# Kernel optimization log

Hardware: AMD Instinct MI355X
Metric: run time of the kernel (lower is better)

## Reference

```python
import jax, jax.numpy as jnp
import numpy as np

LAMBDA_MIN = 0.1
LAMBDA_GLOBAL_MIN = 0.1
LAMBDA_GLOBAL_SCALE = 1.0
SLOPE = 0.2  # negative_slope


def leaky(x):
    return jnp.where(x >= 0, x, SLOPE * x)


def setup_inputs() -> dict:
    key = jax.random.key(0)
    ks = jax.random.split(key, 16)
    n, d, E, C, R = 10000, 128, 320000, 50000, 20
    s = 0.05
    h = jax.random.normal(ks[0], (n, d), jnp.float32)
    edge_index = jax.random.randint(ks[1], (2, E), 0, n)
    edge_type = jax.random.randint(ks[2], (E,), 0, R)
    rel_table = jax.random.normal(ks[3], (R, d), jnp.float32) * s
    # constraints taken from a subset of edges so matches exist
    constraint_indices = edge_index[:, :C]
    constraint_values = jax.random.normal(ks[4], (C,), jnp.float32)
    constraint_types = jax.random.randint(ks[5], (C,), 0, 4)
    att_in = 3 * d  # out*2 + in_dim (use_relation)
    W = jax.random.normal(ks[6], (d, d), jnp.float32) * s
    W_bi = jax.random.normal(ks[7], (d, d), jnp.float32) * s
    att_w1 = jax.random.normal(ks[8], (d, att_in), jnp.float32) * s
    att_b1 = jnp.zeros((d,), jnp.float32)
    att_w2 = jax.random.normal(ks[9], (d,), jnp.float32) * s
    gate_w1 = jax.random.normal(ks[10], (d, 2 * d), jnp.float32) * s
    gate_b1 = jnp.zeros((d,), jnp.float32)
    gate_w2 = jax.random.normal(ks[11], (d,), jnp.float32) * s
    gate_b2 = jnp.zeros((), jnp.float32)
    lambda_c = jnp.full((4,), 0.5, jnp.float32)  # CONSTRAINT_LAMBDA_INIT
    lambda_global = jnp.array(0.5, jnp.float32)
    return dict(h=h, edge_index=edge_index, edge_type=edge_type,
                rel_table=rel_table, constraint_indices=constraint_indices,
                constraint_values=constraint_values, constraint_types=constraint_types,
                W=W, W_bi=W_bi, att_w1=att_w1, att_b1=att_b1, att_w2=att_w2,
                gate_w1=gate_w1, gate_b1=gate_b1, gate_w2=gate_w2, gate_b2=gate_b2,
                lambda_c=lambda_c, lambda_global=lambda_global)


def reference(h, edge_index, edge_type, rel_table, constraint_indices,
              constraint_values, constraint_types, W, W_bi, att_w1, att_b1,
              att_w2, gate_w1, gate_b1, gate_w2, gate_b2, lambda_c, lambda_global):
    n = h.shape[0]
    Wh = h @ W.T                                  # [n, d]
    src, tgt = edge_index[0], edge_index[1]
    src_emb, tgt_emb = Wh[src], Wh[tgt]           # [E, d]
    r_emb = rel_table[edge_type]                  # [E, d]
    att_in = jnp.concatenate([src_emb, tgt_emb, r_emb], axis=-1)  # [E, 3d]
    e = leaky(att_in @ att_w1.T + att_b1) @ att_w2                # [E]

    # ---- constraints (bounded lambdas) ----
    lc = jax.nn.sigmoid(lambda_c) * (1.0 - LAMBDA_MIN) + LAMBDA_MIN
    lg = jax.nn.sigmoid(lambda_global) * (LAMBDA_GLOBAL_SCALE - LAMBDA_GLOBAL_MIN) + LAMBDA_GLOBAL_MIN
    ws = lc[constraint_types] * constraint_values                 # [C]
    c_keys = constraint_indices[0] * n + constraint_indices[1]
    e_keys = src * n + tgt
    # O(n^2) scatter buffers, faithful to the original
    c_agg = jnp.zeros((n * n,), jnp.float32).at[c_keys].add(ws)
    c_exists = jnp.zeros((n * n,), jnp.float32).at[c_keys].add(1.0)
    ms = c_agg[e_keys]
    mask = c_exists[e_keys] > 0
    ms = ms * mask.astype(jnp.float32)
    # constraint gate on matched edges (unmatched entries are 0 anyway)
    gi = jnp.concatenate([src_emb, tgt_emb], axis=-1)             # [E, 2d]
    g = jax.nn.sigmoid(leaky(gi @ gate_w1.T + gate_b1) @ gate_w2 + gate_b2)
    ms = jnp.where(mask, g * ms, ms)
    n_matched = mask.sum()
    global_bias = lg * jnp.mean(ws) * 0.01
    e = jnp.where(n_matched > 0, e + lg * ms, e + global_bias)

    # ---- scatter softmax over src neighborhoods ----
    mx = jax.ops.segment_max(e, src, num_segments=n)
    ex = jnp.exp(jnp.minimum(e - mx[src], 20.0))
    sm = jax.ops.segment_sum(ex, src, num_segments=n)
    attn = ex / (sm[src] + 1e-10)                                 # [E]

    # ---- weighted scatter-add aggregation ----
    side = jax.ops.segment_sum(attn[:, None] * tgt_emb, src, num_segments=n)  # [n, d]

    sum_out = leaky(Wh + side)
    bi_out = leaky((Wh * side) @ W_bi.T)
    h_new = sum_out + bi_out + Wh   # bi-interaction + residual
    return jax.nn.elu(h_new)
```

## Files before the change

### kernel.cpp

```cpp
#include <hip/hip_runtime.h>
#include <stdint.h>

#define SLOPE 0.2f
#define HASH_SIZE 131072
#define POIS ((int)0xAAAAAAAA)
#define MAXDEG 64

typedef __attribute__((ext_vector_type(8))) short bf16x8;
typedef __attribute__((ext_vector_type(4))) float f32x4;

__device__ __forceinline__ float leakyf(float x) { return fmaxf(x, SLOPE * x); }
__device__ __forceinline__ float sigmoidf(float x) { return 1.f / (1.f + __expf(-x)); }
__device__ __forceinline__ unsigned short f2bf(float f) {
  union { float f; unsigned int i; } c; c.f = f;
  unsigned int u = c.i;
  return (unsigned short)((u + 0x7fffu + ((u >> 16) & 1u)) >> 16);
}
__device__ __forceinline__ float bf2f(unsigned short u) {
  union { unsigned int i; float f; } c; c.i = ((unsigned int)u) << 16; return c.f;
}
__device__ __forceinline__ void unpk8(uint4 v, float* o) {
  union { unsigned int i; float f; } t;
  t.i = v.x << 16;          o[0] = t.f;
  t.i = v.x & 0xffff0000u;  o[1] = t.f;
  t.i = v.y << 16;          o[2] = t.f;
  t.i = v.y & 0xffff0000u;  o[3] = t.f;
  t.i = v.z << 16;          o[4] = t.f;
  t.i = v.z & 0xffff0000u;  o[5] = t.f;
  t.i = v.w << 16;          o[6] = t.f;
  t.i = v.w & 0xffff0000u;  o[7] = t.f;
}
__device__ __forceinline__ void ldbf8(const unsigned short* p, float* o) {
  unpk8(*(const uint4*)p, o);
}

__device__ __forceinline__ void mfma_core_a(const bf16x8 (&afr)[4],
                                            const unsigned short* bptr, f32x4 (&acc)[8]) {
  #pragma unroll
  for (int ks = 0; ks < 4; ++ks) {
    #pragma unroll
    for (int ct = 0; ct < 8; ++ct) {
      bf16x8 b = *(const bf16x8*)(bptr + ct * 2048 + ks * 32);
      acc[ct] = __builtin_amdgcn_mfma_f32_16x16x32_bf16(afr[ks], b, acc[ct], 0, 0, 0);
    }
  }
}

__global__ __launch_bounds__(256) void setup_kernel(
    const float* __restrict__ aw1, const float* __restrict__ gw1,
    const float* __restrict__ W, const float* __restrict__ Wbi,
    const float* __restrict__ rel, const float* __restrict__ ab1,
    const int* __restrict__ cidx, const float* __restrict__ cval,
    const int* __restrict__ ctype, const float* __restrict__ lc,
    unsigned short* __restrict__ Wcat, unsigned short* __restrict__ P3b16,
    int* __restrict__ hkeys,
    int C, int n, int R, int H)
{
  int i0 = blockIdx.x * blockDim.x + threadIdx.x;
  int stride = gridDim.x * blockDim.x;
  for (int j = i0; j < 6 * 16384; j += stride) {
    int mat = j >> 14, rest = j & 16383, col = rest >> 7, k = rest & 127;
    float v;
    switch (mat) {
      case 0:  v = aw1[col * 384 + k]; break;
      case 1:  v = aw1[col * 384 + 128 + k]; break;
      case 2:  v = gw1[col * 256 + k]; break;
      case 3:  v = gw1[col * 256 + 128 + k]; break;
      case 4:  v = W[col * 128 + k]; break;
      default: v = Wbi[col * 128 + k]; break;
    }
    Wcat[j] = f2bf(v);
  }
  for (int it = i0; it < R * 128; it += stride) {
    int r = it >> 7, jj = it & 127;
    float acc = ab1[jj];
    const float4* wrow = (const float4*)(aw1 + jj * 384 + 256);
    const float4* rl   = (const float4*)(rel + r * 128);
    #pragma unroll 8
    for (int k = 0; k < 32; ++k) {
      float4 a = rl[k], b = wrow[k];
      acc += a.x * b.x + a.y * b.y + a.z * b.z + a.w * b.w;
    }
    P3b16[it] = f2bf(acc);
  }
  for (int j = i0; j < C; j += stride) {
    int key = cidx[j] * n + cidx[C + j];
    float l = sigmoidf(lc[ctype[j]]) * 0.9f + 0.1f;
    float w = l * cval[j];
    unsigned int slot = ((unsigned int)key * 2654435761u) & (unsigned int)(H - 1);
    while (true) {
      int prev = atomicCAS(&hkeys[2 * slot], POIS, key);
      if (prev == POIS || prev == key) break;
      slot = (slot + 1) & (unsigned int)(H - 1);
    }
    atomicAdd((float*)&hkeys[2 * slot + 1], w);
  }
}

__device__ __forceinline__ void store_tile(const unsigned short (*t)[136],
                                           unsigned short* __restrict__ out,
                                           int rs, int rows_left, int lane)
{
  const int c = (lane & 15) * 8, q = lane >> 4;
  #pragma unroll
  for (int ro = 0; ro < 4; ++ro) {
    int row = ro * 4 + q;
    bf16x8 v = *(const bf16x8*)&t[row][c];
    if (row < rows_left)
      *(bf16x8*)(out + row * rs + c) = v;
  }
}

__global__ __launch_bounds__(256) void gemm_place(
    const int* __restrict__ ei, const int* __restrict__ etype,
    int* __restrict__ cursor, int2* __restrict__ trs2, int E,
    const float* __restrict__ h, const unsigned short* __restrict__ Wcat,
    const int2* __restrict__ hk,
    unsigned short* __restrict__ PW, unsigned short* __restrict__ PQ,
    unsigned short* __restrict__ Q2b,
    int n, int NB5, int H)
{
  if ((int)blockIdx.x >= NB5) {
    int i = ((int)blockIdx.x - NB5) * 256 + threadIdx.x;
    if (i < E) {
      int s = ei[i], t = ei[E + i], rt = etype[i];
      float ms = 0.f;
      int key = s * n + t;
      unsigned int slot = ((unsigned int)key * 2654435761u) & (unsigned int)(H - 1);
      while (true) {
        int2 kv = hk[slot];
        if (kv.x == key) { ms = __int_as_float(kv.y); break; }
        if (kv.x == POIS) break;
        slot = (slot + 1) & (unsigned int)(H - 1);
      }
      int k = atomicAdd(&cursor[s], 1) - POIS;
      if (k < MAXDEG)
        trs2[s * MAXDEG + k] = make_int2(t | (rt << 14), __float_as_int(ms));
    }
    return;
  }
  __shared__ unsigned short tile[4][16][136];
  const int wv = (int)threadIdx.x >> 6, lane = (int)threadIdx.x & 63;
  const int m0 = ((int)blockIdx.x * 4 + wv) * 16;
  if (m0 >= n) return;
  const int r = lane & 15, quad = lane >> 4;
  const int rows_left = n - m0;

  bf16x8 afr[4];
  const float* hrow = h + (size_t)min(m0 + r, n - 1) * 128 + quad * 8;
  #pragma unroll
  for (int ks = 0; ks < 4; ++ks) {
    float4 f0 = *(const float4*)(hrow + ks * 32);
    float4 f1 = *(const float4*)(hrow + ks * 32 + 4);
    bf16x8 a;
    a[0] = (short)f2bf(f0.x); a[1] = (short)f2bf(f0.y);
    a[2] = (short)f2bf(f0.z); a[3] = (short)f2bf(f0.w);
    a[4] = (short)f2bf(f1.x); a[5] = (short)f2bf(f1.y);
    a[6] = (short)f2bf(f1.z); a[7] = (short)f2bf(f1.w);
    afr[ks] = a;
  }

  f32x4 acc[8] = {};
  mfma_core_a(afr, Wcat + 4 * 16384 + r * 128 + quad * 8, acc);
  #pragma unroll
  for (int ct = 0; ct < 8; ++ct)
    #pragma unroll
    for (int rg = 0; rg < 4; ++rg)
      tile[wv][quad * 4 + rg][ct * 16 + r] = f2bf(acc[ct][rg]);

  bf16x8 wfr[4];
  #pragma unroll
  for (int ks = 0; ks < 4; ++ks)
    wfr[ks] = *(const bf16x8*)&tile[wv][r][quad * 8 + ks * 32];

  store_tile(tile[wv], PW + (size_t)m0 * 256 + 128, 256, rows_left, lane);

  #pragma unroll
  for (int mat = 0; mat < 4; ++mat) {
    f32x4 a2[8] = {};
    mfma_core_a(wfr, Wcat + mat * 16384 + r * 128 + quad * 8, a2);
    #pragma unroll
    for (int ct = 0; ct < 8; ++ct)
      #pragma unroll
      for (int rg = 0; rg < 4; ++rg)
        tile[wv][quad * 4 + rg][ct * 16 + r] = f2bf(a2[ct][rg]);
    unsigned short* out; int rs;
    if (mat == 0)      { out = PQ  + (size_t)m0 * 256;        rs = 256; }
    else if (mat == 1) { out = PW  + (size_t)m0 * 256;        rs = 256; }
    else if (mat == 2) { out = PQ  + (size_t)m0 * 256 + 128;  rs = 256; }
    else               { out = Q2b + (size_t)m0 * 128;        rs = 128; }
    store_tile(tile[wv], out, rs, rows_left, lane);
  }
}

__global__ __launch_bounds__(256) void fused_node_wave(
  const int* __restrict__ cursor,
  const int2* __restrict__ trs2,
  const unsigned short* __restrict__ PQ, const unsigned short* __restrict__ PW,
  const unsigned short* __restrict__ P3b16, const unsigned short* __restrict__ Q2,
  const float* __restrict__ aw2, const float* __restrict__ gb1,
  const float* __restrict__ gw2, const float* __restrict__ gb2,
  const float* __restrict__ lgp,
  float* __restrict__ side, unsigned short* __restrict__ Xb16, int n, int R)
{
  __shared__ unsigned short P3l[20 * 128];
  for (int j = threadIdx.x; j < R * 64; j += 256)
    ((unsigned int*)P3l)[j] = ((const unsigned int*)P3b16)[j];
  __syncthreads();

  const int wv = (int)threadIdx.x >> 6;
  const int lane = (int)threadIdx.x & 63;
  const int g = lane >> 4;
  const int u = lane & 15;
  const int d0 = u * 8;

  const int node = (int)blockIdx.x * 4 + wv;
  if (node >= n) return;
  const int cnt = min(cursor[node] - POIS, MAXDEG);
  const int2 ment = trs2[(size_t)node * MAXDEG + lane];

  float p1v[8], w2v[8], qbv[8], g2v[8];
  const unsigned short* pqrow = PQ + (size_t)node * 256 + d0;
  ldbf8(pqrow, p1v);
  { float q1t[8]; ldbf8(pqrow + 128, q1t);
    float4 bA = *(const float4*)(gb1 + d0), bB = *(const float4*)(gb1 + d0 + 4);
    qbv[0]=q1t[0]+bA.x; qbv[1]=q1t[1]+bA.y; qbv[2]=q1t[2]+bA.z; qbv[3]=q1t[3]+bA.w;
    qbv[4]=q1t[4]+bB.x; qbv[5]=q1t[5]+bB.y; qbv[6]=q1t[6]+bB.z; qbv[7]=q1t[7]+bB.w; }
  { float4 a = *(const float4*)(aw2 + d0), b = *(const float4*)(aw2 + d0 + 4);
    w2v[0]=a.x; w2v[1]=a.y; w2v[2]=a.z; w2v[3]=a.w;
    w2v[4]=b.x; w2v[5]=b.y; w2v[6]=b.z; w2v[7]=b.w; }
  { float4 a = *(const float4*)(gw2 + d0), b = *(const float4*)(gw2 + d0 + 4);
    g2v[0]=a.x; g2v[1]=a.y; g2v[2]=a.z; g2v[3]=a.w;
    g2v[4]=b.x; g2v[5]=b.y; g2v[6]=b.z; g2v[7]=b.w; }
  float gb2s = gb2[0];
  float lg = sigmoidf(lgp[0]) * 0.9f + 0.1f;

  float sg = 0.f;
  float acc[8] = {};
  const int iters = (cnt + 3) >> 2;
  const int last = cnt - 1;

  struct Stage { uint4 rpa, rwv, rcc, rq2; float ms; bool act; };

  auto issue = [&](int e0) -> Stage {
    Stage st;
    int e = min(e0, last);
    int bx = __shfl(ment.x, e, 64);
    int by = __shfl(ment.y, e, 64);
    int tx = bx & 16383, rt = (bx >> 14) & 31;
    const unsigned short* pw = PW + (size_t)tx * 256 + d0;
    st.rpa = *(const uint4*)pw;
    st.rwv = *(const uint4*)(pw + 128);
    st.rcc = *(const uint4*)&P3l[rt * 128 + d0];
    st.rq2 = make_uint4(0u, 0u, 0u, 0u);
    if (by != 0) st.rq2 = *(const uint4*)(Q2 + (size_t)tx * 128 + d0);
    st.ms = __int_as_float(by);
    st.act = e0 < cnt;
    return st;
  };

  auto consume = [&](const Stage& st) {
    float pa[8], cc[8];
    unpk8(st.rpa, pa);
    unpk8(st.rcc, cc);
    float s = 0.f;
    #pragma unroll
    for (int d = 0; d < 8; ++d) s += leakyf(p1v[d] + pa[d] + cc[d]) * w2v[d];
    #pragma unroll
    for (int d = 1; d < 16; d <<= 1) s += __shfl_xor(s, d, 64);

    if (st.ms != 0.f) {
      float q2[8];
      unpk8(st.rq2, q2);
      float gp = 0.f;
      #pragma unroll
      for (int d = 0; d < 8; ++d) gp += leakyf(qbv[d] + q2[d]) * g2v[d];
      #pragma unroll
      for (int d = 1; d < 16; d <<= 1) gp += __shfl_xor(gp, d, 64);
      s += lg * (sigmoidf(gp + gb2s) * st.ms);
    }
    if (st.act) {
      float wvv[8];
      unpk8(st.rwv, wvv);
      float p = __expf(s);
      sg += p;
      #pragma unroll
      for (int d = 0; d < 8; ++d) acc[d] += p * wvv[d];
    }
  };

  Stage A = issue(g);
  for (int i = 0; i < iters; ++i) {
    Stage B;
    if (i + 1 < iters) B = issue((i + 1) * 4 + g);
    consume(A);
    A = B;
  }

  sg += __shfl_xor(sg, 16, 64);
  sg += __shfl_xor(sg, 32, 64);
  #pragma unroll
  for (int d = 0; d < 8; ++d) {
    acc[d] += __shfl_xor(acc[d], 16, 64);
    acc[d] += __shfl_xor(acc[d], 32, 64);
  }

  if (g == 0) {
    float inv = 1.f / (sg + 1e-10f);
    int idx = node * 128 + d0;
    float wh[8];
    ldbf8(PW + (size_t)node * 256 + 128 + d0, wh);
    float4 sA = make_float4(acc[0]*inv, acc[1]*inv, acc[2]*inv, acc[3]*inv);
    float4 sB = make_float4(acc[4]*inv, acc[5]*inv, acc[6]*inv, acc[7]*inv);
    *(float4*)(side + idx) = sA;
    *(float4*)(side + idx + 4) = sB;
    ushort4 xA, xB;
    xA.x = f2bf(wh[0] * sA.x); xA.y = f2bf(wh[1] * sA.y);
    xA.z = f2bf(wh[2] * sA.z); xA.w = f2bf(wh[3] * sA.w);
    xB.x = f2bf(wh[4] * sB.x); xB.y = f2bf(wh[5] * sB.y);
    xB.z = f2bf(wh[6] * sB.z); xB.w = f2bf(wh[7] * sB.w);
    *(ushort4*)(Xb16 + idx) = xA;
    *(ushort4*)(Xb16 + idx + 4) = xB;
  }
}

__global__ __launch_bounds__(256) void final_kernel(
    const unsigned short* __restrict__ Xb16, const unsigned short* __restrict__ Wcat,
    int n, const unsigned short* __restrict__ PW, const float* __restrict__ side,
    float* __restrict__ outp)
{
  const int unit = (int)blockIdx.x * 4 + ((int)threadIdx.x >> 6);
  const int tile = unit >> 1, half = unit & 1;
  const int m0 = tile * 16;
  if (m0 >= n) return;
  const int lane = (int)threadIdx.x & 63;
  const int r = lane & 15, quad = lane >> 4;
  int arow = min(m0 + r, n - 1);

  bf16x8 afr[4];
  #pragma unroll
  for (int ks = 0; ks < 4; ++ks)
    afr[ks] = *(const bf16x8*)(Xb16 + (size_t)arow * 128 + quad * 8 + ks * 32);

  const unsigned short* bbase = Wcat + 5 * 16384 + (half * 4) * 2048 + r * 128 + quad * 8;
  f32x4 acc[4] = {};
  #pragma unroll
  for (int ks = 0; ks < 4; ++ks)
    #pragma unroll
    for (int ct = 0; ct < 4; ++ct) {
      bf16x8 b = *(const bf16x8*)(bbase + ct * 2048 + ks * 32);
      acc[ct] = __builtin_amdgcn_mfma_f32_16x16x32_bf16(afr[ks], b, acc[ct], 0, 0, 0);
    }
  #pragma unroll
  for (int ct = 0; ct < 4; ++ct) {
    #pragma unroll
    for (int rg = 0; rg < 4; ++rg) {
      int row = m0 + quad * 4 + rg;
      if (row >= n) continue;
      int col = (half * 4 + ct) * 16 + r;
      int idx = row * 128 + col;
      float v = acc[ct][rg];
      float w = bf2f(PW[(size_t)row * 256 + 128 + col]), s = side[idx];
      float hn = leakyf(w + s) + leakyf(v) + w;
      outp[idx] = hn > 0.f ? hn : __expf(hn) - 1.f;
    }
  }
}

extern "C" void kernel_launch(void* const* d_in, const int* in_sizes, int n_in,
                              void* d_out, int out_size, void* d_ws, size_t ws_size,
                              hipStream_t stream)
{
  const float* h    = (const float*)d_in[0];
  const int* ei     = (const int*)d_in[1];
  const int* etype  = (const int*)d_in[2];
  const float* rel  = (const float*)d_in[3];
  const int* cidx   = (const int*)d_in[4];
  const float* cval = (const float*)d_in[5];
  const int* ctype  = (const int*)d_in[6];
  const float* W    = (const float*)d_in[7];
  const float* Wbi  = (const float*)d_in[8];
  const float* aw1  = (const float*)d_in[9];
  const float* ab1  = (const float*)d_in[10];
  const float* aw2  = (const float*)d_in[11];
  const float* gw1  = (const float*)d_in[12];
  const float* gb1  = (const float*)d_in[13];
  const float* gw2  = (const float*)d_in[14];
  const float* gb2  = (const float*)d_in[15];
  const float* lc   = (const float*)d_in[16];
  const float* lgp  = (const float*)d_in[17];

  const int n = in_sizes[0] / 128;
  const int E = in_sizes[2];
  const int C = in_sizes[6];
  const int R = in_sizes[3] / 128;
  const int H = HASH_SIZE;

  char* ws = (char*)d_ws;
  size_t off = 0;
  auto alloc = [&](size_t bytes) -> void* {
    void* p = ws + off;
    off = (off + bytes + 255) & ~(size_t)255;
    return p;
  };
  unsigned short* PW    = (unsigned short*)alloc((size_t)n * 256 * 2);
  unsigned short* PQ    = (unsigned short*)alloc((size_t)n * 256 * 2);
  unsigned short* Q2b   = (unsigned short*)alloc((size_t)n * 128 * 2);
  unsigned short* Xb16  = (unsigned short*)alloc((size_t)n * 128 * 2);
  unsigned short* Wcat  = (unsigned short*)alloc((size_t)6 * 128 * 128 * 2);
  unsigned short* P3b16 = (unsigned short*)alloc((size_t)R * 128 * 2);
  float* side  = (float*)alloc((size_t)n * 128 * 4);
  int2* trs2   = (int2*)alloc((size_t)n * MAXDEG * 8);
  int* cursor  = (int*)alloc((size_t)n * 4);
  int* hki     = (int*)alloc((size_t)H * 8);
  (void)ws_size; (void)n_in; (void)out_size;

  const int NB5 = (n + 63) / 64;
  const int NBP = (E + 255) / 256;
  const int NB4 = (n + 3) / 4;
  const int NBX = (2 * ((n + 15) / 16) + 3) / 4;

  setup_kernel<<<512, 256, 0, stream>>>(aw1, gw1, W, Wbi, rel, ab1,
                                        cidx, cval, ctype, lc,
                                        Wcat, P3b16, hki, C, n, R, H);
  gemm_place<<<NB5 + NBP, 256, 0, stream>>>(ei, etype, cursor, trs2, E,
                                            h, Wcat, (const int2*)hki,
                                            PW, PQ, Q2b, n, NB5, H);
  fused_node_wave<<<NB4, 256, 0, stream>>>(cursor, trs2, PQ, PW, P3b16, Q2b,
                                           aw2, gb1, gw2, gb2, lgp,
                                           side, Xb16, n, R);
  final_kernel<<<NBX, 256, 0, stream>>>(Xb16, Wcat, n, PW, side, (float*)d_out);
}
```

Baseline: 186.2 us.

## Fuse bi-interaction GEMM and epilogue into the per-node aggregation kernel

The final kernel is merged into the node attention/aggregation kernel. Each block stages its four nodes' Wh*side products (bf16) and the residual terms in shared memory, then runs a small MFMA against W_bi and applies the ELU epilogue directly. This removes the side and Xb16 global buffers and one kernel launch. In exchange, each block reloads the W_bi tile and runs MFMA tiles with only 4 of 16 rows useful.

After: 182.8 us. Within noise of the previous version (-1.9%).

```diff
diff --git a/kernel.cpp b/kernel.cpp
--- a/kernel.cpp
+++ b/kernel.cpp
@@ -15,9 +15,6 @@
   union { float f; unsigned int i; } c; c.f = f;
   unsigned int u = c.i;
   return (unsigned short)((u + 0x7fffu + ((u >> 16) & 1u)) >> 16);
-}
-__device__ __forceinline__ float bf2f(unsigned short u) {
-  union { unsigned int i; float f; } c; c.i = ((unsigned int)u) << 16; return c.f;
 }
 __device__ __forceinline__ void unpk8(uint4 v, float* o) {
   union { unsigned int i; float f; } t;
@@ -193,7 +190,7 @@
   }
 }
 
-__global__ __launch_bounds__(256) void fused_node_wave(
+__global__ __launch_bounds__(256) void fused_node_final(
   const int* __restrict__ cursor,
   const int2* __restrict__ trs2,
   const unsigned short* __restrict__ PQ, const unsigned short* __restrict__ PW,
@@ -201,9 +198,13 @@
   const float* __restrict__ aw2, const float* __restrict__ gb1,
   const float* __restrict__ gw2, const float* __restrict__ gb2,
   const float* __restrict__ lgp,
-  float* __restrict__ side, unsigned short* __restrict__ Xb16, int n, int R)
+  const unsigned short* __restrict__ Wcat5,
+  float* __restrict__ outp, int n, int R)
 {
   __shared__ unsigned short P3l[20 * 128];
+  __shared__ unsigned short Xt[4][136];
+  __shared__ float          Ft[4][132];
+
   for (int j = threadIdx.x; j < R * 64; j += 256)
     ((unsigned int*)P3l)[j] = ((const unsigned int*)P3b16)[j];
   __syncthreads();
@@ -215,154 +216,142 @@
   const int d0 = u * 8;
 
   const int node = (int)blockIdx.x * 4 + wv;
-  if (node >= n) return;
-  const int cnt = min(cursor[node] - POIS, MAXDEG);
-  const int2 ment = trs2[(size_t)node * MAXDEG + lane];
-
-  float p1v[8], w2v[8], qbv[8], g2v[8];
-  const unsigned short* pqrow = PQ + (size_t)node * 256 + d0;
-  ldbf8(pqrow, p1v);
-  { float q1t[8]; ldbf8(pqrow + 128, q1t);
-    float4 bA = *(const float4*)(gb1 + d0), bB = *(const float4*)(gb1 + d0 + 4);
-    qbv[0]=q1t[0]+bA.x; qbv[1]=q1t[1]+bA.y; qbv[2]=q1t[2]+bA.z; qbv[3]=q1t[3]+bA.w;
-    qbv[4]=q1t[4]+bB.x; qbv[5]=q1t[5]+bB.y; qbv[6]=q1t[6]+bB.z; qbv[7]=q1t[7]+bB.w; }
-  { float4 a = *(const float4*)(aw2 + d0), b = *(const float4*)(aw2 + d0 + 4);
-    w2v[0]=a.x; w2v[1]=a.y; w2v[2]=a.z; w2v[3]=a.w;
-    w2v[4]=b.x; w2v[5]=b.y; w2v[6]=b.z; w2v[7]=b.w; }
-  { float4 a = *(const float4*)(gw2 + d0), b = *(const float4*)(gw2 + d0 + 4);
-    g2v[0]=a.x; g2v[1]=a.y; g2v[2]=a.z; g2v[3]=a.w;
-    g2v[4]=b.x; g2v[5]=b.y; g2v[6]=b.z; g2v[7]=b.w; }
-  float gb2s = gb2[0];
-  float lg = sigmoidf(lgp[0]) * 0.9f + 0.1f;
-
-  float sg = 0.f;
-  float acc[8] = {};
-  const int iters = (cnt + 3) >> 2;
-  const int last = cnt - 1;
-
-  struct Stage { uint4 rpa, rwv, rcc, rq2; float ms; bool act; };
-
-  auto issue = [&](int e0) -> Stage {
-    Stage st;
-    int e = min(e0, last);
-    int bx = __shfl(ment.x, e, 64);
-    int by = __shfl(ment.y, e, 64);
-    int tx = bx & 16383, rt = (bx >> 14) & 31;
-    const unsigned short* pw = PW + (size_t)tx * 256 + d0;
-    st.rpa = *(const uint4*)pw;
-    st.rwv = *(const uint4*)(pw + 128);
-    st.rcc = *(const uint4*)&P3l[rt * 128 + d0];
-    st.rq2 = make_uint4(0u, 0u, 0u, 0u);
-    if (by != 0) st.rq2 = *(const uint4*)(Q2 + (size_t)tx * 128 + d0);
-    st.ms = __int_as_float(by);
-    st.act = e0 < cnt;
-    return st;
-  };
-
-  auto consume = [&](const Stage& st) {
-    float pa[8], cc[8];
-    unpk8(st.rpa, pa);
-    unpk8(st.rcc, cc);
-    float s = 0.f;
+  const bool anode = node < n;
+
+  if (anode) {
+    const int cnt = min(cursor[node] - POIS, MAXDEG);
+    const int2 ment = trs2[(size_t)node * MAXDEG + lane];
+
+    float p1v[8], w2v[8], qbv[8], g2v[8];
+    const unsigned short* pqrow = PQ + (size_t)node * 256 + d0;
+    ldbf8(pqrow, p1v);
+    { float q1t[8]; ldbf8(pqrow + 128, q1t);
+      float4 bA = *(const float4*)(gb1 + d0), bB = *(const float4*)(gb1 + d0 + 4);
+      qbv[0]=q1t[0]+bA.x; qbv[1]=q1t[1]+bA.y; qbv[2]=q1t[2]+bA.z; qbv[3]=q1t[3]+bA.w;
+      qbv[4]=q1t[4]+bB.x; qbv[5]=q1t[5]+bB.y; qbv[6]=q1t[6]+bB.z; qbv[7]=q1t[7]+bB.w; }
+    { float4 a = *(const float4*)(aw2 + d0), b = *(const float4*)(aw2 + d0 + 4);
+      w2v[0]=a.x; w2v[1]=a.y; w2v[2]=a.z; w2v[3]=a.w;
+      w2v[4]=b.x; w2v[5]=b.y; w2v[6]=b.z; w2v[7]=b.w; }
+    { float4 a = *(const float4*)(gw2 + d0), b = *(const float4*)(gw2 + d0 + 4);
+      g2v[0]=a.x; g2v[1]=a.y; g2v[2]=a.z; g2v[3]=a.w;
+      g2v[4]=b.x; g2v[5]=b.y; g2v[6]=b.z; g2v[7]=b.w; }
+    float gb2s = gb2[0];
+    float lg = sigmoidf(lgp[0]) * 0.9f + 0.1f;
+
+    float sg = 0.f;
+    float acc[8] = {};
+    const int iters = (cnt + 3) >> 2;
+    const int last = cnt - 1;
+
+    struct Stage { uint4 rpa, rwv, rcc, rq2; float ms; bool act; };
+
+    auto issue = [&](int e0) -> Stage {
+      Stage st;
+      int e = min(e0, last);
+      int bx = __shfl(ment.x, e, 64);
+      int by = __shfl(ment.y, e, 64);
+      int tx = bx & 16383, rt = (bx >> 14) & 31;
+      const unsigned short* pw = PW + (size_t)tx * 256 + d0;
+      st.rpa = *(const uint4*)pw;
+      st.rwv = *(const uint4*)(pw + 128);
+      st.rcc = *(const uint4*)&P3l[rt * 128 + d0];
+      st.rq2 = make_uint4(0u, 0u, 0u, 0u);
+      if (by != 0) st.rq2 = *(const uint4*)(Q2 + (size_t)tx * 128 + d0);
+      st.ms = __int_as_float(by);
+      st.act = e0 < cnt;
+      return st;
+    };
+
+    auto consume = [&](const Stage& st) {
+      float pa[8], cc[8];
+      unpk8(st.rpa, pa);
+      unpk8(st.rcc, cc);
+      float s = 0.f;
+      #pragma unroll
+      for (int d = 0; d < 8; ++d) s += leakyf(p1v[d] + pa[d] + cc[d]) * w2v[d];
+      #pragma unroll
+      for (int d = 1; d < 16; d <<= 1) s += __shfl_xor(s, d, 64);
+
+      if (st.ms != 0.f) {
+        float q2[8];
+        unpk8(st.rq2, q2);
+        float gp = 0.f;
+        #pragma unroll
+        for (int d = 0; d < 8; ++d) gp += leakyf(qbv[d] + q2[d]) * g2v[d];
+        #pragma unroll
+        for (int d = 1; d < 16; d <<= 1) gp += __shfl_xor(gp, d, 64);
+        s += lg * (sigmoidf(gp + gb2s) * st.ms);
+      }
+      if (st.act) {
+        float wvv[8];
+        unpk8(st.rwv, wvv);
+        float p = __expf(s);
+        sg += p;
+        #pragma unroll
+        for (int d = 0; d < 8; ++d) acc[d] += p * wvv[d];
+      }
+    };
+
+    Stage A = issue(g);
+    for (int i = 0; i < iters; ++i) {
+      Stage B;
+      if (i + 1 < iters) B = issue((i + 1) * 4 + g);
+      consume(A);
+      A = B;
+    }
+
+    sg += __shfl_xor(sg, 16, 64);
+    sg += __shfl_xor(sg, 32, 64);
     #pragma unroll
-    for (int d = 0; d < 8; ++d) s += leakyf(p1v[d] + pa[d] + cc[d]) * w2v[d];
-    #pragma unroll
-    for (int d = 1; d < 16; d <<= 1) s += __shfl_xor(s, d, 64);
-
-    if (st.ms != 0.f) {
-      float q2[8];
-      unpk8(st.rq2, q2);
-      float gp = 0.f;
+    for (int d = 0; d < 8; ++d) {
+      acc[d] += __shfl_xor(acc[d], 16, 64);
+      acc[d] += __shfl_xor(acc[d], 32, 64);
+    }
+
+    if (g == 0) {
+      float inv = 1.f / (sg + 1e-10f);
+      float wh[8];
+      ldbf8(PW + (size_t)node * 256 + 128 + d0, wh);
+      bf16x8 xv;
+      float fv[8];
       #pragma unroll
-      for (int d = 0; d < 8; ++d) gp += leakyf(qbv[d] + q2[d]) * g2v[d];
-      #pragma unroll
-      for (int d = 1; d < 16; d <<= 1) gp += __shfl_xor(gp, d, 64);
-      s += lg * (sigmoidf(gp + gb2s) * st.ms);
-    }
-    if (st.act) {
-      float wvv[8];
-      unpk8(st.rwv, wvv);
-      float p = __expf(s);
-      sg += p;
-      #pragma unroll
-      for (int d = 0; d < 8; ++d) acc[d] += p * wvv[d];
-    }
-  };
-
-  Stage A = issue(g);
-  for (int i = 0; i < iters; ++i) {
-    Stage B;
-    if (i + 1 < iters) B = issue((i + 1) * 4 + g);
-    consume(A);
-    A = B;
-  }
-
-  sg += __shfl_xor(sg, 16, 64);
-  sg += __shfl_xor(sg, 32, 64);
-  #pragma unroll
-  for (int d = 0; d < 8; ++d) {
-    acc[d] += __shfl_xor(acc[d], 16, 64);
-    acc[d] += __shfl_xor(acc[d], 32, 64);
-  }
-
+      for (int d = 0; d < 8; ++d) {
+        float sd = acc[d] * inv;
+        xv[d] = (short)f2bf(wh[d] * sd);
+        fv[d] = leakyf(wh[d] + sd) + wh[d];
+      }
+      *(bf16x8*)&Xt[wv][d0] = xv;
+      *(f32x4*)&Ft[wv][d0]     = *(const f32x4*)&fv[0];
+      *(f32x4*)&Ft[wv][d0 + 4] = *(const f32x4*)&fv[4];
+    }
+  }
+  __syncthreads();
+
+  bf16x8 afr2[4];
+  #pragma unroll
+  for (int ks = 0; ks < 4; ++ks)
+    afr2[ks] = *(const bf16x8*)&Xt[u & 3][g * 8 + ks * 32];
+  f32x4 ac0 = {}, ac1 = {};
+  const unsigned short* bb = Wcat5 + (size_t)(wv * 2) * 2048 + u * 128 + g * 8;
+  #pragma unroll
+  for (int ks = 0; ks < 4; ++ks) {
+    bf16x8 b0 = *(const bf16x8*)(bb + ks * 32);
+    bf16x8 b1 = *(const bf16x8*)(bb + 2048 + ks * 32);
+    ac0 = __builtin_amdgcn_mfma_f32_16x16x32_bf16(afr2[ks], b0, ac0, 0, 0, 0);
+    ac1 = __builtin_amdgcn_mfma_f32_16x16x32_bf16(afr2[ks], b1, ac1, 0, 0, 0);
+  }
   if (g == 0) {
-    float inv = 1.f / (sg + 1e-10f);
-    int idx = node * 128 + d0;
-    float wh[8];
-    ldbf8(PW + (size_t)node * 256 + 128 + d0, wh);
-    float4 sA = make_float4(acc[0]*inv, acc[1]*inv, acc[2]*inv, acc[3]*inv);
-    float4 sB = make_float4(acc[4]*inv, acc[5]*inv, acc[6]*inv, acc[7]*inv);
-    *(float4*)(side + idx) = sA;
-    *(float4*)(side + idx + 4) = sB;
-    ushort4 xA, xB;
-    xA.x = f2bf(wh[0] * sA.x); xA.y = f2bf(wh[1] * sA.y);
-    xA.z = f2bf(wh[2] * sA.z); xA.w = f2bf(wh[3] * sA.w);
-    xB.x = f2bf(wh[4] * sB.x); xB.y = f2bf(wh[5] * sB.y);
-    xB.z = f2bf(wh[6] * sB.z); xB.w = f2bf(wh[7] * sB.w);
-    *(ushort4*)(Xb16 + idx) = xA;
-    *(ushort4*)(Xb16 + idx + 4) = xB;
-  }
-}
-
-__global__ __launch_bounds__(256) void final_kernel(
-    const unsigned short* __restrict__ Xb16, const unsigned short* __restrict__ Wcat,
-    int n, const unsigned short* __restrict__ PW, const float* __restrict__ side,
-    float* __restrict__ outp)
-{
-  const int unit = (int)blockIdx.x * 4 + ((int)threadIdx.x >> 6);
-  const int tile = unit >> 1, half = unit & 1;
-  const int m0 = tile * 16;
-  if (m0 >= n) return;
-  const int lane = (int)threadIdx.x & 63;
-  const int r = lane & 15, quad = lane >> 4;
-  int arow = min(m0 + r, n - 1);
-
-  bf16x8 afr[4];
-  #pragma unroll
-  for (int ks = 0; ks < 4; ++ks)
-    afr[ks] = *(const bf16x8*)(Xb16 + (size_t)arow * 128 + quad * 8 + ks * 32);
-
-  const unsigned short* bbase = Wcat + 5 * 16384 + (half * 4) * 2048 + r * 128 + quad * 8;
-  f32x4 acc[4] = {};
-  #pragma unroll
-  for (int ks = 0; ks < 4; ++ks)
-    #pragma unroll
-    for (int ct = 0; ct < 4; ++ct) {
-      bf16x8 b = *(const bf16x8*)(bbase + ct * 2048 + ks * 32);
-      acc[ct] = __builtin_amdgcn_mfma_f32_16x16x32_bf16(afr[ks], b, acc[ct], 0, 0, 0);
-    }
-  #pragma unroll
-  for (int ct = 0; ct < 4; ++ct) {
+    const int base = (int)blockIdx.x * 4;
+    const int c0 = wv * 32 + u, c1 = c0 + 16;
     #pragma unroll
     for (int rg = 0; rg < 4; ++rg) {
-      int row = m0 + quad * 4 + rg;
-      if (row >= n) continue;
-      int col = (half * 4 + ct) * 16 + r;
-      int idx = row * 128 + col;
-      float v = acc[ct][rg];
-      float w = bf2f(PW[(size_t)row * 256 + 128 + col]), s = side[idx];
-      float hn = leakyf(w + s) + leakyf(v) + w;
-      outp[idx] = hn > 0.f ? hn : __expf(hn) - 1.f;
+      int nrow = base + rg;
+      if (nrow < n) {
+        float hn0 = Ft[rg][c0] + leakyf(ac0[rg]);
+        float hn1 = Ft[rg][c1] + leakyf(ac1[rg]);
+        outp[(size_t)nrow * 128 + c0] = hn0 > 0.f ? hn0 : __expf(hn0) - 1.f;
+        outp[(size_t)nrow * 128 + c1] = hn1 > 0.f ? hn1 : __expf(hn1) - 1.f;
+      }
     }
   }
 }
@@ -406,10 +395,8 @@
   unsigned short* PW    = (unsigned short*)alloc((size_t)n * 256 * 2);
   unsigned short* PQ    = (unsigned short*)alloc((size_t)n * 256 * 2);
   unsigned short* Q2b   = (unsigned short*)alloc((size_t)n * 128 * 2);
-  unsigned short* Xb16  = (unsigned short*)alloc((size_t)n * 128 * 2);
   unsigned short* Wcat  = (unsigned short*)alloc((size_t)6 * 128 * 128 * 2);
   unsigned short* P3b16 = (unsigned short*)alloc((size_t)R * 128 * 2);
-  float* side  = (float*)alloc((size_t)n * 128 * 4);
   int2* trs2   = (int2*)alloc((size_t)n * MAXDEG * 8);
   int* cursor  = (int*)alloc((size_t)n * 4);
   int* hki     = (int*)alloc((size_t)H * 8);
@@ -418,7 +405,6 @@
   const int NB5 = (n + 63) / 64;
   const int NBP = (E + 255) / 256;
   const int NB4 = (n + 3) / 4;
-  const int NBX = (2 * ((n + 15) / 16) + 3) / 4;
 
   setup_kernel<<<512, 256, 0, stream>>>(aw1, gw1, W, Wbi, rel, ab1,
                                         cidx, cval, ctype, lc,
@@ -426,8 +412,7 @@
   gemm_place<<<NB5 + NBP, 256, 0, stream>>>(ei, etype, cursor, trs2, E,
                                             h, Wcat, (const int2*)hki,
                                             PW, PQ, Q2b, n, NB5, H);
-  fused_node_wave<<<NB4, 256, 0, stream>>>(cursor, trs2, PQ, PW, P3b16, Q2b,
-                                           aw2, gb1, gw2, gb2, lgp,
-                                           side, Xb16, n, R);
-  final_kernel<<<NBX, 256, 0, stream>>>(Xb16, Wcat, n, PW, side, (float*)d_out);
-}
+  fused_node_final<<<NB4, 256, 0, stream>>>(cursor, trs2, PQ, PW, P3b16, Q2b,
+                                            aw2, gb1, gw2, gb2, lgp,
+                                            Wcat + 5 * 16384, (float*)d_out, n, R);
+}
```
